# Kernel tuning notes

Measured on AMD Instinct MI355X. Metric: run time of the kernel, lower is better.

Reference implementation:

```python
import jax, jax.numpy as jnp
import numpy as np

GAMMA = 0.99
EPS = 1e-05
K = 8192   # num_embeddings
D = 256    # embed_dim
B, T = 32, 1024

def setup_inputs() -> dict:
    key = jax.random.key(0)
    k1, k2 = jax.random.split(key)
    ze = jax.random.normal(k1, (B, T, D), dtype=jnp.float32)
    embedW = jax.random.normal(k2, (K, D), dtype=jnp.float32)
    mt = jnp.zeros((K, D), dtype=jnp.float32)
    Nt = jnp.zeros((K,), dtype=jnp.float32)
    return {"ze": ze, "embedW": embedW, "mt": mt, "Nt": Nt}

def reference(ze, embedW, mt, Nt):
    b = ze.shape[0]
    ze_flat = ze.reshape(-1, ze.shape[-1])                      # [N, D]
    # squared euclidean distances: ||z||^2 - 2 z W^T + ||w||^2  -> [N, K]
    dist_mat = (jnp.sum(ze_flat * ze_flat, axis=1, keepdims=True)
                - 2.0 * ze_flat @ embedW.T
                + jnp.sum(embedW * embedW, axis=1)[None, :])
    zq_idx = jnp.argmin(dist_mat, axis=-1)                      # [N]
    zq = embedW[zq_idx]                                         # gather [N, D]
    # EMA codebook update (training mode), one-hot scatter expressed as segment sums
    nt = jax.ops.segment_sum(jnp.ones_like(zq_idx, dtype=jnp.float32), zq_idx, num_segments=K)
    Nt_new = GAMMA * Nt + (1.0 - GAMMA) * nt
    st = jax.ops.segment_sum(ze_flat, zq_idx, num_segments=K)   # one_hot.T @ ze
    mt_new = GAMMA * mt + (1.0 - GAMMA) * st
    n = jnp.sum(Nt_new)
    Nn = (Nt_new + EPS) * n / (n + K * EPS)
    embedW_new = mt_new / Nn[:, None]
    zq = zq.reshape(b, -1, zq.shape[-1])                        # [B, T, D]
    zq_idx = zq_idx.reshape(b, -1)                              # [B, T]
    commit = jnp.mean((jax.lax.stop_gradient(zq) - ze) ** 2)
    zq_st = ze + jax.lax.stop_gradient(zq - ze)                 # straight-through
    return (zq_st, commit, zq_idx, embedW_new, mt_new, Nt_new)
```

## Files before the change

### kernel.cpp

```cpp
#include <hip/hip_runtime.h>
#include <cstddef>
#include <cstdint>

#define GAMMA_F 0.99f
#define OMG_F   0.01f
#define EPS_F   1e-5f
#define KN 8192
#define DD 256
#define NN 32768

#define OFF_ZQ     0
#define OFF_COMMIT 8388608
#define OFF_IDX    8388609
#define OFF_EMB    8421377
#define OFF_MT     10518529
#define OFF_NT     12615681

#define C1 32
#define NCH1 (NN / C1)
#define NREC (NCH1 * 2)
#define C2 32
#define NCH2 (NREC / C2)

typedef _Float16 half8 __attribute__((ext_vector_type(8)));
typedef _Float16 half4 __attribute__((ext_vector_type(4)));
typedef float    f32x4 __attribute__((ext_vector_type(4)));
typedef unsigned long long u64;

__device__ __forceinline__ void gload16(const void* g, void* l) {
    __builtin_amdgcn_global_load_lds(
        (const __attribute__((address_space(1))) unsigned int*)g,
        (__attribute__((address_space(3))) unsigned int*)l, 16, 0, 0);
}

__device__ __forceinline__ u64 packdi(float dist, int n) {
    unsigned u = __float_as_uint(dist);
    u ^= (unsigned)((int)u >> 31) | 0x80000000u;
    return ((u64)u << 32) | (unsigned)n;
}

__global__ __launch_bounds__(256) void conv_hi_kernel(
    const float* __restrict__ x, _Float16* __restrict__ hi) {
    const size_t i0 = ((size_t)blockIdx.x * 256 + threadIdx.x) * 4;
    const float4 v = *(const float4*)(x + i0);
    half4 h;
    h[0] = (_Float16)v.x; h[1] = (_Float16)v.y;
    h[2] = (_Float16)v.z; h[3] = (_Float16)v.w;
    *(half4*)(hi + i0) = h;
}

__global__ __launch_bounds__(64) void convw_wsq_kernel(
    const float* __restrict__ W, _Float16* __restrict__ wh,
    float* __restrict__ wsq) {
    const int k = blockIdx.x;
    const int lane = threadIdx.x;
    const float4 v = *(const float4*)(W + (size_t)k * DD + lane * 4);
    half4 h;
    h[0] = (_Float16)v.x; h[1] = (_Float16)v.y;
    h[2] = (_Float16)v.z; h[3] = (_Float16)v.w;
    *(half4*)(wh + (size_t)k * DD + lane * 4) = h;
    float s = v.x * v.x + v.y * v.y + v.z * v.z + v.w * v.w;
#pragma unroll
    for (int off = 32; off > 0; off >>= 1) s += __shfl_down(s, off, 64);
    if (lane == 0) wsq[k] = s;
}

__global__ __launch_bounds__(512, 2) void screen_kernel(
    const _Float16* __restrict__ zh, const _Float16* __restrict__ wh,
    const float* __restrict__ wsq, u64* __restrict__ tmin2) {
    __shared__ __align__(16) _Float16 As[2][256 * 64];
    __shared__ __align__(16) _Float16 Bs[2][256 * 64];
    __shared__ __align__(16) u64 top2[256][4];

    const int tid  = threadIdx.x;
    const int wave = tid >> 6;
    const int lane = tid & 63;
    const int quad = lane >> 4;
    const int col  = lane & 15;
    const int ph = wave >> 2;
    const int cq = wave & 3;

    const int bm = blockIdx.x >> 5;
    const int bn = blockIdx.x & 31;
    const int m0 = bm * 256;
    const int n0 = bn * 256;

    f32x4 acc[4][8];
#pragma unroll
    for (int i = 0; i < 4; i++)
#pragma unroll
        for (int j = 0; j < 8; j++) acc[i][j] = (f32x4){0.f, 0.f, 0.f, 0.f};

    auto stage = [&](int b, int c) {
        const int d0 = c * 64;
#pragma unroll
        for (int t = 0; t < 4; ++t) {
            const int clin = (wave * 4 + t) * 64 + lane;
            const int mrow = clin >> 3;
            const int q = (clin & 7) ^ (mrow & 7);
            gload16(zh + (size_t)(m0 + mrow) * DD + d0 + q * 8,
                    &As[b][(wave * 4 + t) * 512]);
            gload16(wh + (size_t)(n0 + mrow) * DD + d0 + q * 8,
                    &Bs[b][(wave * 4 + t) * 512]);
        }
    };

    stage(0, 0);
    __syncthreads();

    for (int c = 0; c < 4; ++c) {
        if (c < 3) stage((c + 1) & 1, c + 1);
        const _Float16* Ab = As[c & 1];
        const _Float16* Bb = Bs[c & 1];
#pragma unroll
        for (int kk = 0; kk < 2; ++kk) {
            half8 a[4], b[8];
            const int cc = kk * 4 + quad;
#pragma unroll
            for (int t = 0; t < 4; ++t) {
                const int cr = cq * 64 + t * 16 + col;
                a[t] = *(const half8*)(Bb + cr * 64 + (cc ^ (cr & 7)) * 8);
            }
#pragma unroll
            for (int t = 0; t < 8; ++t) {
                const int pr = ph * 128 + t * 16 + col;
                b[t] = *(const half8*)(Ab + pr * 64 + (cc ^ (pr & 7)) * 8);
            }
#pragma unroll
            for (int ci = 0; ci < 4; ++ci)
#pragma unroll
                for (int pj = 0; pj < 8; ++pj)
                    acc[ci][pj] = __builtin_amdgcn_mfma_f32_16x16x32_f16(
                        a[ci], b[pj], acc[ci][pj], 0, 0, 0);
        }
        __syncthreads();
    }

    float wq[4][4];
#pragma unroll
    for (int ci = 0; ci < 4; ++ci) {
        const float4 t =
            *(const float4*)(wsq + n0 + cq * 64 + ci * 16 + quad * 4);
        wq[ci][0] = t.x + 4096.f; wq[ci][1] = t.y + 4096.f;
        wq[ci][2] = t.z + 4096.f; wq[ci][3] = t.w + 4096.f;
    }
    const unsigned base7 = (unsigned)((cq & 1) * 64 + quad * 4);

#pragma unroll
    for (int pj = 0; pj < 8; ++pj) {
        unsigned t0 = 0xFFFFFFFFu, t1 = 0xFFFFFFFFu;
#pragma unroll
        for (int ci = 0; ci < 4; ++ci)
#pragma unroll
            for (int v = 0; v < 4; ++v) {
                const float dist = fmaf(-2.0f, acc[ci][pj][v], wq[ci][v]);
                const unsigned x = (__float_as_uint(dist) & ~127u) |
                                   (base7 + ci * 16 + v);
                const unsigned mx = t0 > x ? t0 : x;
                t0 = t0 < x ? t0 : x;
                t1 = t1 < mx ? t1 : mx;
            }
#pragma unroll
        for (int mk = 16; mk < 64; mk <<= 1) {
            const unsigned o0 = __shfl_xor(t0, mk, 64);
            const unsigned o1 = __shfl_xor(t1, mk, 64);
            const unsigned lo = t0 < o0 ? t0 : o0;
            const unsigned hi = t0 < o0 ? o0 : t0;
            const unsigned mn = t1 < o1 ? t1 : o1;
            t0 = lo;
            t1 = hi < mn ? hi : mn;
        }
        if (quad == 0)
            top2[ph * 128 + pj * 16 + col][cq] = ((u64)t1 << 32) | t0;
    }
    __syncthreads();
    {
        const int p = tid & 255;
        const int h = tid >> 8;
        const u64 e0 = top2[p][2 * h], e1 = top2[p][2 * h + 1];
        const unsigned a0 = (unsigned)e0, a1 = (unsigned)(e0 >> 32);
        const unsigned b0 = (unsigned)e1, b1 = (unsigned)(e1 >> 32);
        const unsigned t0 = a0 < b0 ? a0 : b0;
        const unsigned hi = a0 < b0 ? b0 : a0;
        const unsigned mn = a1 < b1 ? a1 : b1;
        const unsigned t1 = hi < mn ? hi : mn;
        const unsigned c1 = n0 + h * 128 + (t0 & 127u);
        const unsigned c2 = n0 + h * 128 + (t1 & 127u);
        const u64 ent = (u64)(t0 & ~127u) | ((u64)c1 << 32) | ((u64)c2 << 48);
        tmin2[(size_t)(bn * 2 + h) * NN + m0 + p] = ent;
    }
}

__global__ __launch_bounds__(256) void compact_kernel(
    const u64* __restrict__ tmin2,
    unsigned* __restrict__ cnt, unsigned* __restrict__ slots,
    unsigned* __restrict__ hist_zero,
    const float* __restrict__ mt_in, float* __restrict__ mt_out) {
    const int tid = threadIdx.x;
    const int gid = blockIdx.x * 256 + tid;
    if (gid < KN) hist_zero[gid] = 0u;
    if (gid < KN * DD / 4) {
        const float4 m = *(const float4*)(mt_in + (size_t)gid * 4);
        float4 r;
        r.x = GAMMA_F * m.x; r.y = GAMMA_F * m.y;
        r.z = GAMMA_F * m.z; r.w = GAMMA_F * m.w;
        *(float4*)(mt_out + (size_t)gid * 4) = r;
    }

    const int lane = tid & 63;
    const int n = blockIdx.x * 4 + (tid >> 6);
    const u64 e = tmin2[(size_t)lane * NN + n];
    const float d1 = __uint_as_float((unsigned)e);
    float mn = d1;
#pragma unroll
    for (int off = 32; off > 0; off >>= 1)
        mn = fminf(mn, __shfl_xor(mn, off, 64));
    const bool q = d1 <= mn + 1.0f;
    const u64 bal = __ballot(q);
    if (q) {
        const int rank = __popcll(bal & ((1ull << lane) - 1ull));
        if (rank < 16) {
            slots[(size_t)n * 32 + 2 * rank + 0] = (unsigned)(e >> 32) & 0xffffu;
            slots[(size_t)n * 32 + 2 * rank + 1] = (unsigned)(e >> 48);
        }
    }
    if (lane == 0) {
        unsigned c = 2u * (unsigned)__popcll(bal);
        cnt[n] = c < 32u ? c : 32u;
    }
}

__global__ __launch_bounds__(256) void rescore_gather_kernel(
    const float* __restrict__ ze, const float* __restrict__ W,
    const unsigned* __restrict__ cnt, const unsigned* __restrict__ slots,
    float* __restrict__ idxf, float* __restrict__ zq_out,
    unsigned* __restrict__ hist, float* __restrict__ partials) {
    const int tid = threadIdx.x;
    const int lane = tid & 63;
    const int n = blockIdx.x * 4 + (tid >> 6);
    const float4 z = *(const float4*)(ze + (size_t)n * DD + lane * 4);
    const unsigned m = cnt[n];
    u64 best = ~0ull;
    for (unsigned j = 0; j < m; ++j) {
        const unsigned c = slots[(size_t)n * 32 + j];
        const float4 w = *(const float4*)(W + (size_t)c * DD + lane * 4);
        float dot = z.x * w.x + z.y * w.y + z.z * w.z + z.w * w.w;
        float wq  = w.x * w.x + w.y * w.y + w.z * w.z + w.w * w.w;
#pragma unroll
        for (int off = 32; off > 0; off >>= 1) {
            dot += __shfl_xor(dot, off, 64);
            wq  += __shfl_xor(wq, off, 64);
        }
        const float dist = fmaf(-2.0f, dot, wq);
        const u64 pk = packdi(dist, (int)c);
        best = best < pk ? best : pk;
    }
    const int idx = (int)(unsigned)(best & 0xFFFFFFFFull);
    if (lane == 0) {
        idxf[n] = (float)idx;
        atomicAdd(hist + idx, 1u);
    }

    const float4 w = *(const float4*)(W + (size_t)idx * DD + lane * 4);
    float4 d, o;
    d.x = w.x - z.x; d.y = w.y - z.y; d.z = w.z - z.z; d.w = w.w - z.w;
    o.x = z.x + d.x; o.y = z.y + d.y; o.z = z.z + d.z; o.w = z.w + d.w;
    *(float4*)(zq_out + (size_t)n * DD + lane * 4) = o;

    float c = d.x * d.x + d.y * d.y + d.z * d.z + d.w * d.w;
#pragma unroll
    for (int off = 32; off > 0; off >>= 1) c += __shfl_down(c, off, 64);

    __shared__ float wsum[4];
    if (lane == 0) wsum[tid >> 6] = c;
    __syncthreads();
    if (tid == 0)
        partials[blockIdx.x] = wsum[0] + wsum[1] + wsum[2] + wsum[3];
}

__global__ __launch_bounds__(256) void prefix_kernel(
    const float* __restrict__ Nt_in, float* __restrict__ ntn,
    const float* __restrict__ partials, float* __restrict__ commit_out,
    unsigned* __restrict__ offsets) {
    const int t = threadIdx.x;
    unsigned* hist = (unsigned*)ntn;
    const int base = t * 32;
    unsigned loc[32];
    unsigned sum = 0;
#pragma unroll
    for (int i = 0; i < 32; ++i) { loc[i] = hist[base + i]; sum += loc[i]; }

    __shared__ unsigned ssum[256];
    __shared__ float cred[256];
    ssum[t] = sum;
    float cp = 0.f;
    for (int i = t; i < NN / 4; i += 256) cp += partials[i];
    cred[t] = cp;
    __syncthreads();

    for (int off = 1; off < 256; off <<= 1) {
        const unsigned v = (t >= off) ? ssum[t - off] : 0u;
        __syncthreads();
        ssum[t] += v;
        __syncthreads();
    }
    unsigned run = (t > 0) ? ssum[t - 1] : 0u;

    for (int off = 128; off > 0; off >>= 1) {
        if (t < off) cred[t] += cred[t + off];
        __syncthreads();
    }
    if (t == 0) *commit_out = cred[0] * (1.0f / 8388608.0f);

#pragma unroll
    for (int i = 0; i < 32; ++i) {
        offsets[base + i] = run;
        run += loc[i];
    }
#pragma unroll
    for (int i = 0; i < 32; ++i)
        ntn[base + i] = GAMMA_F * Nt_in[base + i] + OMG_F * (float)loc[i];
}

__global__ __launch_bounds__(256) void scatter_kernel(
    const float* __restrict__ idxf, unsigned* __restrict__ offsets,
    unsigned* __restrict__ perm, unsigned* __restrict__ codes) {
    const int n = blockIdx.x * 256 + threadIdx.x;
    const int idx = (int)idxf[n];
    const unsigned pos = atomicAdd(offsets + idx, 1u);
    perm[pos] = n;
    codes[pos] = (unsigned)idx;
}

__global__ __launch_bounds__(256) void mt1_kernel(
    const float* __restrict__ ze, const float* __restrict__ mt_in,
    const unsigned* __restrict__ perm, const unsigned* __restrict__ codes,
    float* __restrict__ mt_out, unsigned* __restrict__ prec,
    float* __restrict__ pdata) {
    const int tid = threadIdx.x;
    const int lane = tid & 63;
    const int w = blockIdx.x * 4 + (tid >> 6);
    const int j0 = w * C1;

    unsigned ccur = codes[j0];
    bool first = true;
    float4 acc = {0.f, 0.f, 0.f, 0.f};

    for (int j = j0; j < j0 + C1; ++j) {
        const unsigned c = codes[j];
        if (c != ccur) {
            if (first) {
                *(float4*)(pdata + (size_t)(2 * w) * DD + lane * 4) = acc;
                if (lane == 0) prec[2 * w] = ccur;
                first = false;
            } else {
                const size_t o = (size_t)ccur * DD + lane * 4;
                const float4 m = *(const float4*)(mt_in + o);
                float4 r;
                r.x = GAMMA_F * m.x + OMG_F * acc.x;
                r.y = GAMMA_F * m.y + OMG_F * acc.y;
                r.z = GAMMA_F * m.z + OMG_F * acc.z;
                r.w = GAMMA_F * m.w + OMG_F * acc.w;
                *(float4*)(mt_out + o) = r;
            }
            acc = (float4){0.f, 0.f, 0.f, 0.f};
            ccur = c;
        }
        const unsigned p = perm[j];
        const float4 z = *(const float4*)(ze + (size_t)p * DD + lane * 4);
        acc.x += z.x; acc.y += z.y; acc.z += z.z; acc.w += z.w;
    }
    if (first) {
        *(float4*)(pdata + (size_t)(2 * w) * DD + lane * 4) = acc;
        *(float4*)(pdata + (size_t)(2 * w + 1) * DD + lane * 4) =
            (float4){0.f, 0.f, 0.f, 0.f};
        if (lane == 0) { prec[2 * w] = ccur; prec[2 * w + 1] = ccur; }
    } else {
        *(float4*)(pdata + (size_t)(2 * w + 1) * DD + lane * 4) = acc;
        if (lane == 0) prec[2 * w + 1] = ccur;
    }
}

__global__ __launch_bounds__(256) void mt2_kernel(
    const float* __restrict__ mt_in, const unsigned* __restrict__ prec,
    const float* __restrict__ pdata, float* __restrict__ mt_out) {
    const int tid = threadIdx.x;
    const int lane = tid & 63;
    const int w = blockIdx.x * 4 + (tid >> 6);
    const int r0 = w * C2;

    unsigned ccur = prec[r0];
    bool first = true;
    float4 acc = {0.f, 0.f, 0.f, 0.f};

    for (int r = r0; r < r0 + C2; ++r) {
        const unsigned c = prec[r];
        if (c != ccur) {
            if (first) {
                float* mp = mt_out + (size_t)ccur * DD + lane * 4;
                atomicAdd(mp + 0, OMG_F * acc.x);
                atomicAdd(mp + 1, OMG_F * acc.y);
                atomicAdd(mp + 2, OMG_F * acc.z);
                atomicAdd(mp + 3, OMG_F * acc.w);
                first = false;
            } else {
                const size_t o = (size_t)ccur * DD + lane * 4;
                const float4 m = *(const float4*)(mt_in + o);
                float4 rr;
                rr.x = GAMMA_F * m.x + OMG_F * acc.x;
                rr.y = GAMMA_F * m.y + OMG_F * acc.y;
                rr.z = GAMMA_F * m.z + OMG_F * acc.z;
                rr.w = GAMMA_F * m.w + OMG_F * acc.w;
                *(float4*)(mt_out + o) = rr;
            }
            acc = (float4){0.f, 0.f, 0.f, 0.f};
            ccur = c;
        }
        const float4 v = *(const float4*)(pdata + (size_t)r * DD + lane * 4);
        acc.x += v.x; acc.y += v.y; acc.z += v.z; acc.w += v.w;
    }
    float* mp = mt_out + (size_t)ccur * DD + lane * 4;
    atomicAdd(mp + 0, OMG_F * acc.x);
    atomicAdd(mp + 1, OMG_F * acc.y);
    atomicAdd(mp + 2, OMG_F * acc.z);
    atomicAdd(mp + 3, OMG_F * acc.w);
}

__global__ __launch_bounds__(256) void final_kernel(
    const float* __restrict__ nt_new, const float* __restrict__ mt_new,
    float* __restrict__ emb_out) {
    __shared__ float red[256];
    float s = 0.0f;
    for (int i = threadIdx.x; i < KN; i += 256) s += nt_new[i];
    red[threadIdx.x] = s;
    __syncthreads();
    for (int off = 128; off > 0; off >>= 1) {
        if (threadIdx.x < off) red[threadIdx.x] += red[threadIdx.x + off];
        __syncthreads();
    }
    const float n = red[0];

    const size_t i0 = ((size_t)blockIdx.x * 256 + threadIdx.x) * 4;
    const int k = (int)(i0 >> 8);

    const float4 mt = *(const float4*)(mt_new + i0);
    const float Nn = (nt_new[k] + EPS_F) * n / (n + (float)KN * EPS_F);
    float4 e;
    e.x = mt.x / Nn;
    e.y = mt.y / Nn;
    e.z = mt.z / Nn;
    e.w = mt.w / Nn;
    *(float4*)(emb_out + i0) = e;
}

extern "C" void kernel_launch(void* const* d_in, const int* in_sizes, int n_in,
                              void* d_out, int out_size, void* d_ws, size_t ws_size,
                              hipStream_t stream) {
    const float* ze = (const float*)d_in[0];
    const float* W  = (const float*)d_in[1];
    const float* mt = (const float*)d_in[2];
    const float* Nt = (const float*)d_in[3];

    float* out    = (float*)d_out;
    float* zq_out = out + OFF_ZQ;
    float* commit = out + OFF_COMMIT;
    float* idxf   = out + OFF_IDX;
    float* emb    = out + OFF_EMB;
    float* mtn    = out + OFF_MT;
    float* ntn    = out + OFF_NT;

    _Float16* zh = (_Float16*)zq_out;
    u64* tmin2 =
        (u64*)(zq_out + (size_t)NN * DD / 2);
    _Float16* wh = (_Float16*)(mtn + 3);
    float* wsqbuf = idxf + 3;
    unsigned* cnt      = (unsigned*)emb;
    unsigned* slots    = cnt + NN;
    float*    partials = (float*)(slots + (size_t)NN * 32);
    unsigned* offsets  = (unsigned*)partials + NN / 4;
    unsigned* perm     = offsets + KN;
    unsigned* codes    = perm + NN;
    unsigned* prec     = codes + NN;
    float*    pdata    = (float*)(prec + NREC);
    unsigned* hist     = (unsigned*)ntn;

    conv_hi_kernel<<<(NN * DD / 4) / 256, 256, 0, stream>>>(ze, zh);
    convw_wsq_kernel<<<KN, 64, 0, stream>>>(W, wh, wsqbuf);

    screen_kernel<<<(NN / 256) * (KN / 256), 512, 0, stream>>>(
        zh, wh, wsqbuf, tmin2);

    compact_kernel<<<NN / 4, 256, 0, stream>>>(tmin2, cnt, slots, hist,
                                               mt, mtn);

    rescore_gather_kernel<<<NN / 4, 256, 0, stream>>>(
        ze, W, cnt, slots, idxf, zq_out, hist, partials);

    prefix_kernel<<<1, 256, 0, stream>>>(Nt, ntn, partials, commit, offsets);

    scatter_kernel<<<NN / 256, 256, 0, stream>>>(idxf, offsets, perm, codes);

    mt1_kernel<<<NCH1 / 4, 256, 0, stream>>>(ze, mt, perm, codes, mtn,
                                             prec, pdata);

    mt2_kernel<<<NCH2 / 4, 256, 0, stream>>>(mt, prec, pdata, mtn);

    final_kernel<<<(KN * DD / 4) / 256, 256, 0, stream>>>(ntn, mtn, emb);
}
```

Measured before the change: 391.1 us.

## Deepen screen GEMM pipeline to four 32-wide LDS stages with swizzled block order

Splits the D=256 reduction into eight 32-wide chunks held in a 4-deep LDS ring, prefetching three chunks ahead and waiting with explicit vmcnt counts and raw s_barrier instead of full __syncthreads. It also remaps block IDs so consecutive blocks spread across the M dimension, aiming for better L2 reuse of codebook tiles, and raises wave priority around the MFMA burst. The goal is to hide global-load latency behind matrix math. The cost is more barriers per tile and hand-counted waitcnt values, which break if the number of loads per stage changes.

Result: slower. 422.8 us (+8.1%).

```diff
diff --git a/kernel.cpp b/kernel.cpp
--- a/kernel.cpp
+++ b/kernel.cpp
@@ -68,8 +68,8 @@
 __global__ __launch_bounds__(512, 2) void screen_kernel(
     const _Float16* __restrict__ zh, const _Float16* __restrict__ wh,
     const float* __restrict__ wsq, u64* __restrict__ tmin2) {
-    __shared__ __align__(16) _Float16 As[2][256 * 64];
-    __shared__ __align__(16) _Float16 Bs[2][256 * 64];
+    __shared__ __align__(16) _Float16 As[4][256 * 32];
+    __shared__ __align__(16) _Float16 Bs[4][256 * 32];
     __shared__ __align__(16) u64 top2[256][4];
 
     const int tid  = threadIdx.x;
@@ -80,8 +80,9 @@
     const int ph = wave >> 2;
     const int cq = wave & 3;
 
-    const int bm = blockIdx.x >> 5;
-    const int bn = blockIdx.x & 31;
+    const int vid = ((blockIdx.x & 7) << 9) | (blockIdx.x >> 3);
+    const int bm = vid >> 5;
+    const int bn = vid & 31;
     const int m0 = bm * 256;
     const int n0 = bn * 256;
 
@@ -91,50 +92,68 @@
 #pragma unroll
         for (int j = 0; j < 8; j++) acc[i][j] = (f32x4){0.f, 0.f, 0.f, 0.f};
 
-    auto stage = [&](int b, int c) {
-        const int d0 = c * 64;
-#pragma unroll
-        for (int t = 0; t < 4; ++t) {
-            const int clin = (wave * 4 + t) * 64 + lane;
-            const int mrow = clin >> 3;
-            const int q = (clin & 7) ^ (mrow & 7);
-            gload16(zh + (size_t)(m0 + mrow) * DD + d0 + q * 8,
-                    &As[b][(wave * 4 + t) * 512]);
-            gload16(wh + (size_t)(n0 + mrow) * DD + d0 + q * 8,
-                    &Bs[b][(wave * 4 + t) * 512]);
+    auto stage = [&](int c) {
+        const int b = c & 3;
+        const int d0 = c * 32;
+#pragma unroll
+        for (int t = 0; t < 2; ++t) {
+            const int r = wave * 2 + t;
+            const int row = r * 16 + (lane >> 2);
+            const int g = (lane & 3) ^ ((row & 3) ^ ((row >> 2) & 3));
+            gload16(zh + (size_t)(m0 + row) * DD + d0 + g * 8,
+                    &As[b][r * 512]);
+            gload16(wh + (size_t)(n0 + row) * DD + d0 + g * 8,
+                    &Bs[b][r * 512]);
         }
     };
 
-    stage(0, 0);
-    __syncthreads();
-
-    for (int c = 0; c < 4; ++c) {
-        if (c < 3) stage((c + 1) & 1, c + 1);
-        const _Float16* Ab = As[c & 1];
-        const _Float16* Bb = Bs[c & 1];
-#pragma unroll
-        for (int kk = 0; kk < 2; ++kk) {
-            half8 a[4], b[8];
-            const int cc = kk * 4 + quad;
-#pragma unroll
-            for (int t = 0; t < 4; ++t) {
-                const int cr = cq * 64 + t * 16 + col;
-                a[t] = *(const half8*)(Bb + cr * 64 + (cc ^ (cr & 7)) * 8);
-            }
-#pragma unroll
-            for (int t = 0; t < 8; ++t) {
-                const int pr = ph * 128 + t * 16 + col;
-                b[t] = *(const half8*)(Ab + pr * 64 + (cc ^ (pr & 7)) * 8);
-            }
-#pragma unroll
-            for (int ci = 0; ci < 4; ++ci)
-#pragma unroll
-                for (int pj = 0; pj < 8; ++pj)
-                    acc[ci][pj] = __builtin_amdgcn_mfma_f32_16x16x32_f16(
-                        a[ci], b[pj], acc[ci][pj], 0, 0, 0);
-        }
-        __syncthreads();
-    }
+    stage(0); stage(1); stage(2);
+    asm volatile("s_waitcnt vmcnt(8)" ::: "memory");
+    __builtin_amdgcn_s_barrier();
+    __builtin_amdgcn_sched_barrier(0);
+
+#define DO_CHUNK(C, DO_STAGE, VMWAIT, DO_SYNC)                               \
+    {                                                                         \
+        if (DO_STAGE) stage((C) + 3);                                         \
+        const _Float16* Ab = As[(C) & 3];                                     \
+        const _Float16* Bb = Bs[(C) & 3];                                     \
+        half8 a[4], b[8];                                                     \
+        _Pragma("unroll")                                                     \
+        for (int t = 0; t < 4; ++t) {                                         \
+            const int cr = cq * 64 + t * 16 + col;                            \
+            const int sl = quad ^ ((cr & 3) ^ ((cr >> 2) & 3));               \
+            a[t] = *(const half8*)(Bb + cr * 32 + sl * 8);                    \
+        }                                                                     \
+        _Pragma("unroll")                                                     \
+        for (int t = 0; t < 8; ++t) {                                         \
+            const int pr = ph * 128 + t * 16 + col;                           \
+            const int sl = quad ^ ((pr & 3) ^ ((pr >> 2) & 3));               \
+            b[t] = *(const half8*)(Ab + pr * 32 + sl * 8);                    \
+        }                                                                     \
+        __builtin_amdgcn_s_setprio(1);                                        \
+        _Pragma("unroll")                                                     \
+        for (int ci = 0; ci < 4; ++ci)                                        \
+            _Pragma("unroll")                                                 \
+            for (int pj = 0; pj < 8; ++pj)                                    \
+                acc[ci][pj] = __builtin_amdgcn_mfma_f32_16x16x32_f16(         \
+                    a[ci], b[pj], acc[ci][pj], 0, 0, 0);                      \
+        __builtin_amdgcn_s_setprio(0);                                        \
+        if (DO_SYNC) {                                                        \
+            asm volatile("s_waitcnt vmcnt(" VMWAIT ")" ::: "memory");         \
+            __builtin_amdgcn_s_barrier();                                     \
+            __builtin_amdgcn_sched_barrier(0);                                \
+        }                                                                     \
+    }
+
+    DO_CHUNK(0, true,  "8", true)
+    DO_CHUNK(1, true,  "8", true)
+    DO_CHUNK(2, true,  "8", true)
+    DO_CHUNK(3, true,  "8", true)
+    DO_CHUNK(4, true,  "8", true)
+    DO_CHUNK(5, false, "4", true)
+    DO_CHUNK(6, false, "0", true)
+    DO_CHUNK(7, false, "0", false)
+#undef DO_CHUNK
 
     float wq[4][4];
 #pragma unroll
```
